# Optimization experiments

Hardware: AMD Instinct MI355X
Metric: run time of the kernel (lower is better)

## Reference

```python
import jax, jax.numpy as jnp
import numpy as np

B, T, S = 64, 32, 64          # batch, tgt_len, src_len
V, E, H, C = 32000, 512, 1024, 2048  # vocab, emb, hidden, context (2*d_model)


def setup_inputs() -> dict:
    key = jax.random.key(0)
    ks = jax.random.split(key, 16)
    g = lambda i, shape, s=0.05: jax.random.normal(ks[i], shape, jnp.float32) * s
    return dict(
        y=jax.random.randint(ks[0], (B, T), 0, V),
        context=g(1, (B, S, C), 1.0),
        context_mask=jnp.zeros((B, S), jnp.int32),  # 1 = padding
        hidden=g(2, (B, H), 1.0),
        emb=g(3, (V, E)),
        W_ih1=g(4, (3 * H, E)), W_hh1=g(5, (3 * H, H)),
        b_ih1=jnp.zeros((3 * H,), jnp.float32), b_hh1=jnp.zeros((3 * H,), jnp.float32),
        Wq=g(6, (H, H)), bq=jnp.zeros((H,), jnp.float32),
        Wk=g(7, (C, H)), v_attn=g(8, (H,)),
        W_ih2=g(9, (3 * H, C)), W_hh2=g(10, (3 * H, H)),
        b_ih2=jnp.zeros((3 * H,), jnp.float32), b_hh2=jnp.zeros((3 * H,), jnp.float32),
        Wi=g(11, (E, E)), bi=jnp.zeros((E,), jnp.float32),
        Wh=g(12, (E, H)), bh=jnp.zeros((E,), jnp.float32),
        Wc=g(13, (E, C)), bc=jnp.zeros((E,), jnp.float32),
    )


def gru_cell(x, h, W_ih, W_hh, b_ih, b_hh):
    gi = x @ W_ih.T + b_ih
    gh = h @ W_hh.T + b_hh
    i_r, i_z, i_n = jnp.split(gi, 3, axis=-1)
    h_r, h_z, h_n = jnp.split(gh, 3, axis=-1)
    r = jax.nn.sigmoid(i_r + h_r)
    z = jax.nn.sigmoid(i_z + h_z)
    n = jnp.tanh(i_n + r * h_n)
    return (1.0 - z) * n + z * h


def reference(y, context, context_mask, hidden, emb,
              W_ih1, W_hh1, b_ih1, b_hh1,
              Wq, bq, Wk, v_attn,
              W_ih2, W_hh2, b_ih2, b_hh2,
              Wi, bi, Wh, bh, Wc, bc):
    x = emb[y]                                        # [B,T,E]
    cache = jnp.einsum('bsc,ch->bsh', context, Wk)    # attention key cache
    pad = context_mask.astype(bool)
    neg = jnp.finfo(x.dtype).min

    def step(h, x_t):
        h1 = gru_cell(x_t, h, W_ih1, W_hh1, b_ih1, b_hh1)        # [B,H]
        q = h1 @ Wq + bq                                          # [B,H]
        scores = jnp.einsum('bsh,h->bs', jnp.tanh(q[:, None, :] + cache), v_attn)
        probs = jax.nn.softmax(jnp.where(pad, neg, scores), axis=-1)
        attn = jnp.einsum('bs,bsc->bc', probs, context)           # [B,C]
        h2 = gru_cell(attn, h1, W_ih2, W_hh2, b_ih2, b_hh2)
        return h2, (h2, attn)

    h_final, (out, attn) = jax.lax.scan(step, hidden, jnp.swapaxes(x, 0, 1))
    out = jnp.swapaxes(out, 0, 1)                     # [B,T,H]
    attn = jnp.swapaxes(attn, 0, 1)                   # [B,T,C]
    logits = jnp.tanh(x @ Wi.T + bi + out @ Wh.T + bh + attn @ Wc.T + bc)
    return logits, h_final
```

## Files before the change

kernel.cpp:

```cpp
#include <hip/hip_runtime.h>
#include <math.h>

#define B_ 64
#define T_ 32
#define S_ 64
#define E_ 512
#define H_ 1024
#define C_ 2048
#define G_ 3072
#define NBLK 256
#define FLSTR 16

typedef __bf16 bf16_t;
typedef bf16_t bf16x8 __attribute__((ext_vector_type(8)));
typedef float f32x4 __attribute__((ext_vector_type(4)));
typedef unsigned long long u64;

__device__ __forceinline__ float sigm_(float x) { return 1.f / (1.f + __expf(-x)); }
__device__ __forceinline__ float tanh_(float x) { return 1.f - 2.f / (__expf(2.f * x) + 1.f); }

__device__ __forceinline__ unsigned short bits_(bf16_t x)
{
    union { bf16_t b; unsigned short u; } c; c.b = x; return c.u;
}
__device__ __forceinline__ void astore_pair(bf16_t* p, bf16_t lo, bf16_t hi)
{
    unsigned u = (unsigned)bits_(lo) | ((unsigned)bits_(hi) << 16);
    __hip_atomic_store((unsigned*)p, u, __ATOMIC_RELAXED, __HIP_MEMORY_SCOPE_AGENT);
}
__device__ __forceinline__ void astore_f32(float* p, float v)
{
    union { float f; unsigned u; } c; c.f = v;
    __hip_atomic_store((unsigned*)p, c.u, __ATOMIC_RELAXED, __HIP_MEMORY_SCOPE_AGENT);
}
__device__ __forceinline__ void astore_2f32(float* p, float a, float b)
{
    union { float f[2]; u64 u; } c; c.f[0] = a; c.f[1] = b;
    __hip_atomic_store((u64*)p, c.u, __ATOMIC_RELAXED, __HIP_MEMORY_SCOPE_AGENT);
}

__device__ __forceinline__ void split8(const float* __restrict__ p, bf16x8& h, bf16x8& l)
{
    float4 a = *(const float4*)p;
    float4 b = *(const float4*)(p + 4);
    float v[8] = {a.x, a.y, a.z, a.w, b.x, b.y, b.z, b.w};
    #pragma unroll
    for (int q = 0; q < 8; ++q) {
        h[q] = (bf16_t)v[q];
        l[q] = (bf16_t)(v[q] - (float)h[q]);
    }
}

__global__ __launch_bounds__(256)
void embed_kernel(const int* __restrict__ y, const float* __restrict__ emb,
                  float* __restrict__ x)
{
    int i = blockIdx.x * 256 + threadIdx.x;
    int row = i / (E_ / 4);
    int e4  = i % (E_ / 4);
    const float4* src = (const float4*)(emb + (size_t)y[row] * E_);
    ((float4*)(x + (size_t)row * E_))[e4] = src[e4];
}

__global__ void transpose_kernel(const float* __restrict__ in, float* __restrict__ out,
                                 int R, int Ccols)
{
    __shared__ float t[32][33];
    int r0 = blockIdx.y * 32, c0 = blockIdx.x * 32;
    t[threadIdx.y][threadIdx.x] = in[(size_t)(r0 + threadIdx.y) * Ccols + c0 + threadIdx.x];
    __syncthreads();
    out[(size_t)(c0 + threadIdx.y) * R + r0 + threadIdx.x] = t[threadIdx.x][threadIdx.y];
}

__global__ __launch_bounds__(256)
void cvt_ctx(const float* __restrict__ in, bf16_t* __restrict__ out)
{
    int i = blockIdx.x * 256 + threadIdx.x;
    const float4* s4 = (const float4*)in + 2 * i;
    float4 a = s4[0], b = s4[1];
    bf16x8 o;
    o[0] = (bf16_t)a.x; o[1] = (bf16_t)a.y; o[2] = (bf16_t)a.z; o[3] = (bf16_t)a.w;
    o[4] = (bf16_t)b.x; o[5] = (bf16_t)b.y; o[6] = (bf16_t)b.z; o[7] = (bf16_t)b.w;
    ((bf16x8*)out)[i] = o;
}

#define LSTR 80

template<int ACCUM>
__global__ __launch_bounds__(256)
void sgemm(const float* __restrict__ A, const float* __restrict__ Wt,
           float* __restrict__ out, int N, int K)
{
    __shared__ char AH[128 * LSTR];
    __shared__ char AL[128 * LSTR];
    __shared__ char WH[128 * LSTR];
    __shared__ char WL[128 * LSTR];
    const int tid = threadIdx.x;
    const int lane = tid & 63, wave = tid >> 6;
    const int m0 = blockIdx.y * 128, n0 = blockIdx.x * 128;
    const int wm = (wave & 1) * 64, wn = (wave >> 1) * 64;
    const int l15 = lane & 15, l4 = lane >> 4;

    f32x4 acc[4][4] = {};

    for (int k0 = 0; k0 < K; k0 += 32) {
        #pragma unroll
        for (int p = 0; p < 2; ++p) {
            int e = tid + p * 256;
            int row = e >> 2, ch = e & 3;
            int off = row * LSTR + ch * 16;
            bf16x8 h, l;
            split8(A + (size_t)(m0 + row) * K + k0 + ch * 8, h, l);
            *(bf16x8*)(AH + off) = h; *(bf16x8*)(AL + off) = l;
            split8(Wt + (size_t)(n0 + row) * K + k0 + ch * 8, h, l);
            *(bf16x8*)(WH + off) = h; *(bf16x8*)(WL + off) = l;
        }
        __syncthreads();
        bf16x8 ah[4], al[4], wh[4], wl[4];
        #pragma unroll
        for (int i = 0; i < 4; ++i) {
            int off = (wm + i * 16 + l15) * LSTR + l4 * 16;
            ah[i] = *(const bf16x8*)(AH + off);
            al[i] = *(const bf16x8*)(AL + off);
        }
        #pragma unroll
        for (int j = 0; j < 4; ++j) {
            int off = (wn + j * 16 + l15) * LSTR + l4 * 16;
            wh[j] = *(const bf16x8*)(WH + off);
            wl[j] = *(const bf16x8*)(WL + off);
        }
        #pragma unroll
        for (int i = 0; i < 4; ++i)
            #pragma unroll
            for (int j = 0; j < 4; ++j) {
                acc[i][j] = __builtin_amdgcn_mfma_f32_16x16x32_bf16(ah[i], wh[j], acc[i][j], 0, 0, 0);
                acc[i][j] = __builtin_amdgcn_mfma_f32_16x16x32_bf16(ah[i], wl[j], acc[i][j], 0, 0, 0);
                acc[i][j] = __builtin_amdgcn_mfma_f32_16x16x32_bf16(al[i], wh[j], acc[i][j], 0, 0, 0);
            }
        __syncthreads();
    }

    #pragma unroll
    for (int i = 0; i < 4; ++i)
        #pragma unroll
        for (int j = 0; j < 4; ++j)
            #pragma unroll
            for (int r = 0; r < 4; ++r) {
                int m = m0 + wm + i * 16 + l4 * 4 + r;
                int n = n0 + wn + j * 16 + l15;
                if (ACCUM) out[(size_t)m * N + n] += acc[i][j][r];
                else       out[(size_t)m * N + n]  = acc[i][j][r];
            }
}

#define W1H_OFF 0
#define W1L_OFF 24576
#define W3H_OFF 49152
#define W2H_OFF 98304
#define W2L_OFF 131072
#define SMEM_BYTES 163840

__device__ __forceinline__ void gbar(unsigned* flags, unsigned* done,
                                     unsigned epoch, int blk, int tid)
{
    asm volatile("s_waitcnt vmcnt(0)" ::: "memory");
    __syncthreads();
    if (blk == 0) {
        if (tid > 0 && tid < NBLK) {
            while (__hip_atomic_load(&flags[tid * FLSTR], __ATOMIC_RELAXED,
                                     __HIP_MEMORY_SCOPE_AGENT) < epoch)
                __builtin_amdgcn_s_sleep(4);
        }
        __syncthreads();
        if (tid < 8)
            __hip_atomic_store(&done[tid * FLSTR], epoch, __ATOMIC_RELAXED,
                               __HIP_MEMORY_SCOPE_AGENT);
        __syncthreads();
    } else {
        if (tid == 0) {
            __hip_atomic_store(&flags[blk * FLSTR], epoch, __ATOMIC_RELAXED,
                               __HIP_MEMORY_SCOPE_AGENT);
            while (__hip_atomic_load(&done[(blk & 7) * FLSTR], __ATOMIC_RELAXED,
                                     __HIP_MEMORY_SCOPE_AGENT) < epoch)
                __builtin_amdgcn_s_sleep(4);
        }
        __syncthreads();
    }
}

__global__ __launch_bounds__(1024, 1)
void scan_kernel(
    const float* __restrict__ Whh1, const float* __restrict__ Whh2,
    const float* __restrict__ WqT,  const float* __restrict__ Wih2,
    const float* __restrict__ Xg,
    const float* __restrict__ b_ih1, const float* __restrict__ b_hh1,
    const float* __restrict__ b_ih2, const float* __restrict__ b_hh2,
    const float* __restrict__ bq,    const float* __restrict__ v_attn,
    const int*   __restrict__ cmask,
    const float* __restrict__ hidden,
    const float* __restrict__ cacheK, const bf16_t* __restrict__ ctxb,
    float* __restrict__ qgv, float* __restrict__ hf,
    bf16_t* __restrict__ h1H, bf16_t* __restrict__ h1L,
    float* __restrict__ attnseq, float* __restrict__ outseq,
    float* __restrict__ hfinal,
    float* __restrict__ scgv,
    unsigned* __restrict__ flags, unsigned* __restrict__ done)
{
    extern __shared__ char sm[];
    const int tid = threadIdx.x, blk = blockIdx.x;
    const int lane = tid & 63, wave = tid >> 6;
    const int l15 = lane & 15, l4 = lane >> 4;
    const int blk4 = blk * 4;
    const int ab  = blk & 63;
    const int aq  = blk >> 6;

    if (tid == 0) __builtin_amdgcn_fence(__ATOMIC_ACQUIRE, "agent");
    __syncthreads();

    for (int e = tid; e < 12 * 128; e += 1024) {
        int r = e >> 7, c = e & 127;
        bf16x8 h, l;
        split8(Whh1 + (size_t)((r >> 2) * 1024 + blk4 + (r & 3)) * 1024 + c * 8, h, l);
        int off = r * 2048 + ((c * 16) ^ ((r & 7) << 4));
        *(bf16x8*)(sm + W1H_OFF + off) = h;
        *(bf16x8*)(sm + W1L_OFF + off) = l;
    }
    for (int e = tid; e < 16 * 128; e += 1024) {
        int r = e >> 7, c = e & 127;
        const float* src = (r < 12)
            ? Whh2 + (size_t)((r >> 2) * 1024 + blk4 + (r & 3)) * 1024 + c * 8
            : WqT + (size_t)(blk4 + r - 12) * 1024 + c * 8;
        bf16x8 h, l;
        split8(src, h, l);
        int off = r * 2048 + ((c * 16) ^ ((r & 7) << 4));
        *(bf16x8*)(sm + W2H_OFF + off) = h;
        *(bf16x8*)(sm + W2L_OFF + off) = l;
    }
    for (int e = tid; e < 12 * 256; e += 1024) {
        int r = e >> 8, c = e & 255;
        bf16x8 h, l;
        split8(Wih2 + (size_t)((r >> 2) * 1024 + blk4 + (r & 3)) * 2048 + c * 8, h, l);
        *(bf16x8*)(sm + W3H_OFF + r * 4096 + ((c * 16) ^ ((r & 7) << 4))) = h;
    }

    const int j = blk4 + l15;
    if (wave < 4 && l15 < 4) {
        #pragma unroll
        for (int r2 = 0; r2 < 4; ++r2) {
            int b = wave * 16 + l4 * 4 + r2;
            hf[b * 1024 + j] = hidden[b * 1024 + j];
        }
    }

    float vreg[16], bqreg[16];
    #pragma unroll
    for (int i = 0; i < 16; ++i) {
        vreg[i]  = v_attn[lane + 64 * i];
        bqreg[i] = bq[lane + 64 * i];
    }

    float bi1r = 0, bi1z = 0, bi1n = 0, bh1r = 0, bh1z = 0, bh1n = 0;
    float bi2r = 0, bi2z = 0, bi2n = 0, bh2r = 0, bh2z = 0, bh2n = 0;
    if (wave < 4 && l15 < 4) {
        bi1r = b_ih1[j]; bi1z = b_ih1[1024 + j]; bi1n = b_ih1[2048 + j];
        bh1r = b_hh1[j]; bh1z = b_hh1[1024 + j]; bh1n = b_hh1[2048 + j];
        bi2r = b_ih2[j]; bi2z = b_ih2[1024 + j]; bi2n = b_ih2[2048 + j];
        bh2r = b_hh2[j]; bh2z = b_hh2[1024 + j]; bh2n = b_hh2[2048 + j];
    }

    unsigned epoch = 0;
    gbar(flags, done, ++epoch, blk, tid);

    float h1r_[4] = {0.f, 0.f, 0.f, 0.f};
    f32x4 acc1 = {0.f, 0.f, 0.f, 0.f};

    for (int t = 0; t < T_; ++t) {
        if (wave < 4) {
            f32x4 acc0 = {0.f, 0.f, 0.f, 0.f};
            const int brow = wave * 16 + l15;
            const float* asrc = (t == 0) ? hidden + (size_t)brow * 1024
                                         : outseq + ((size_t)brow * T_ + t - 1) * 1024;
            #pragma unroll 8
            for (int kk = 0; kk < 32; ++kk) {
                bf16x8 avh, avl;
                split8(asrc + kk * 32 + l4 * 8, avh, avl);
                int boff = (kk * 64 + l4 * 16) ^ ((l15 & 7) << 4);
                bf16x8 bvh = *(const bf16x8*)(sm + W1H_OFF + l15 * 2048 + boff);
                bf16x8 bvl = *(const bf16x8*)(sm + W1L_OFF + l15 * 2048 + boff);
                acc0 = __builtin_amdgcn_mfma_f32_16x16x32_bf16(avh, bvh, acc0, 0, 0, 0);
                acc0 = __builtin_amdgcn_mfma_f32_16x16x32_bf16(avl, bvh, acc0, 0, 0, 0);
                acc0 = __builtin_amdgcn_mfma_f32_16x16x32_bf16(avh, bvl, acc0, 0, 0, 0);
            }
            #pragma unroll
            for (int r2 = 0; r2 < 4; ++r2) {
                float gr = acc0[r2];
                float gz = __shfl(acc0[r2], (lane & 48) | (l15 + 4), 64);
                float gn = __shfl(acc0[r2], (lane & 48) | (l15 + 8), 64);
                float h1v = 0.f;
                int b = wave * 16 + l4 * 4 + r2;
                if (l15 < 4) {
                    const float* xg = Xg + ((size_t)b * T_ + t) * 3072;
                    float rr = sigm_(xg[j]          + bi1r + gr + bh1r);
                    float zz = sigm_(xg[1024 + j]   + bi1z + gz + bh1z);
                    float nn = tanh_(xg[2048 + j]   + bi1n + rr * (gn + bh1n));
                    h1v = (1.f - zz) * nn + zz * hf[b * 1024 + j];
                    h1r_[r2] = h1v;
                }
                float h1o = __shfl(h1v, lane + 1, 64);
                if (l15 < 4 && (l15 & 1) == 0) {
                    bf16_t hS = (bf16_t)h1v, hO = (bf16_t)h1o;
                    size_t vo = ((size_t)t * 64 + b) * 1024 + j;
                    astore_pair(h1H + vo, hS, hO);
                    astore_pair(h1L + vo,
                                (bf16_t)(h1v - (float)hS), (bf16_t)(h1o - (float)hO));
                }
            }
        }
        gbar(flags, done, ++epoch, blk, tid);

        if (wave < 4) {
            acc1 = (f32x4){0.f, 0.f, 0.f, 0.f};
            const int brow = wave * 16 + l15;
            const bf16_t* ah = h1H + ((size_t)t * 64 + brow) * 1024;
            const bf16_t* al = h1L + ((size_t)t * 64 + brow) * 1024;
            #pragma unroll 8
            for (int kk = 0; kk < 32; ++kk) {
                bf16x8 avh = *(const bf16x8*)(ah + kk * 32 + l4 * 8);
                bf16x8 avl = *(const bf16x8*)(al + kk * 32 + l4 * 8);
                int boff = (kk * 64 + l4 * 16) ^ ((l15 & 7) << 4);
                bf16x8 bvh = *(const bf16x8*)(sm + W2H_OFF + l15 * 2048 + boff);
                bf16x8 bvl = *(const bf16x8*)(sm + W2L_OFF + l15 * 2048 + boff);
                acc1 = __builtin_amdgcn_mfma_f32_16x16x32_bf16(avh, bvh, acc1, 0, 0, 0);
                acc1 = __builtin_amdgcn_mfma_f32_16x16x32_bf16(avl, bvh, acc1, 0, 0, 0);
                acc1 = __builtin_amdgcn_mfma_f32_16x16x32_bf16(avh, bvl, acc1, 0, 0, 0);
            }
            if (l15 >= 12) {
                int jq = blk4 + l15 - 12;
                #pragma unroll
                for (int r2 = 0; r2 < 4; ++r2)
                    astore_f32(&qgv[((size_t)t * 64 + (wave * 16 + l4 * 4 + r2)) * 1024 + jq],
                               acc1[r2]);
            }
        }
        gbar(flags, done, ++epoch, blk, tid);

        {
            int s = aq * 16 + wave;
            const float* qrow = qgv + ((size_t)t * 64 + ab) * 1024;
            const float* ck = cacheK + ((size_t)ab * 64 + s) * 1024;
            float sum = 0.f;
            #pragma unroll
            for (int i = 0; i < 16; ++i)
                sum += tanh_(qrow[lane + 64 * i] + bqreg[i] + ck[lane + 64 * i]) * vreg[i];
            #pragma unroll
            for (int off = 32; off; off >>= 1) sum += __shfl_down(sum, off, 64);
            if (lane == 0) astore_f32(&scgv[(size_t)t * 4096 + ab * 64 + s], sum);
        }
        gbar(flags, done, ++epoch, blk, tid);

        if (tid < 256) {
            const float* scrow = scgv + (size_t)t * 4096 + ab * 64;
            float v = (cmask[ab * 64 + lane] != 0) ? -3.4e38f : scrow[lane];
            float mx = v;
            #pragma unroll
            for (int off = 32; off; off >>= 1) mx = fmaxf(mx, __shfl_xor(mx, off, 64));
            float e = __expf(v - mx);
            float sden = e;
            #pragma unroll
            for (int off = 32; off; off >>= 1) sden += __shfl_xor(sden, off, 64);
            float prv = e / sden;

            int c = aq * 512 + tid * 2;
            const bf16_t* cb = ctxb + (size_t)ab * 64 * 2048 + c;
            float sum0 = 0.f, sum1 = 0.f;
            #pragma unroll 8
            for (int s = 0; s < 64; ++s) {
                float p = __shfl(prv, s, 64);
                bf16_t v0 = cb[(size_t)s * 2048];
                bf16_t v1 = cb[(size_t)s * 2048 + 1];
                sum0 += p * (float)v0;
                sum1 += p * (float)v1;
            }
            astore_2f32(attnseq + ((size_t)ab * T_ + t) * 2048 + c, sum0, sum1);
        }
        gbar(flags, done, ++epoch, blk, tid);

        if (wave < 4) {
            f32x4 acc3 = {0.f, 0.f, 0.f, 0.f};
            const int brow = wave * 16 + l15;
            const float* aptr = attnseq + ((size_t)brow * T_ + t) * 2048;
            #pragma unroll 8
            for (int kk = 0; kk < 64; ++kk) {
                bf16x8 avh, avl;
                split8(aptr + kk * 32 + l4 * 8, avh, avl);
                bf16x8 bvh = *(const bf16x8*)(sm + W3H_OFF + l15 * 4096 +
                                              ((kk * 64 + l4 * 16) ^ ((l15 & 7) << 4)));
                acc3 = __builtin_amdgcn_mfma_f32_16x16x32_bf16(avh, bvh, acc3, 0, 0, 0);
                acc3 = __builtin_amdgcn_mfma_f32_16x16x32_bf16(avl, bvh, acc3, 0, 0, 0);
            }
            #pragma unroll
            for (int r2 = 0; r2 < 4; ++r2) {
                float ir  = acc3[r2];
                float iz  = __shfl(acc3[r2], (lane & 48) | (l15 + 4), 64);
                float in2 = __shfl(acc3[r2], (lane & 48) | (l15 + 8), 64);
                float hr  = acc1[r2];
                float hz  = __shfl(acc1[r2], (lane & 48) | (l15 + 4), 64);
                float hn  = __shfl(acc1[r2], (lane & 48) | (l15 + 8), 64);
                int b = wave * 16 + l4 * 4 + r2;
                if (l15 < 4) {
                    float rr = sigm_(ir + bi2r + hr + bh2r);
                    float zz = sigm_(iz + bi2z + hz + bh2z);
                    float nn = tanh_(in2 + bi2n + rr * (hn + bh2n));
                    float h2 = (1.f - zz) * nn + zz * h1r_[r2];
                    hf[b * 1024 + j] = h2;
                    astore_f32(&outseq[((size_t)b * T_ + t) * 1024 + j], h2);
                    if (t == T_ - 1) hfinal[b * 1024 + j] = h2;
                }
            }
        }
        gbar(flags, done, ++epoch, blk, tid);
    }
}

__global__ __launch_bounds__(256)
void final_kernel(const float* __restrict__ Lacc,
                  const float* __restrict__ bi, const float* __restrict__ bh,
                  const float* __restrict__ bc, float* __restrict__ out)
{
    int i = blockIdx.x * 256 + threadIdx.x;
    int e = i & 511;
    out[i] = tanh_(Lacc[i] + bi[e] + bh[e] + bc[e]);
}

extern "C" void kernel_launch(void* const* d_in, const int* in_sizes, int n_in,
                              void* d_out, int out_size, void* d_ws, size_t ws_size,
                              hipStream_t stream)
{
    const int*   y       = (const int*)  d_in[0];
    const float* context = (const float*)d_in[1];
    const int*   cmask   = (const int*)  d_in[2];
    const float* hidden  = (const float*)d_in[3];
    const float* emb     = (const float*)d_in[4];
    const float* W_ih1   = (const float*)d_in[5];
    const float* W_hh1   = (const float*)d_in[6];
    const float* b_ih1   = (const float*)d_in[7];
    const float* b_hh1   = (const float*)d_in[8];
    const float* Wq      = (const float*)d_in[9];
    const float* bq      = (const float*)d_in[10];
    const float* Wk      = (const float*)d_in[11];
    const float* v_attn  = (const float*)d_in[12];
    const float* W_ih2   = (const float*)d_in[13];
    const float* W_hh2   = (const float*)d_in[14];
    const float* b_ih2   = (const float*)d_in[15];
    const float* b_hh2   = (const float*)d_in[16];
    const float* Wi      = (const float*)d_in[17];
    const float* bi      = (const float*)d_in[18];
    const float* Wh      = (const float*)d_in[19];
    const float* bh      = (const float*)d_in[20];
    const float* Wc      = (const float*)d_in[21];
    const float* bc      = (const float*)d_in[22];

    char* ws = (char*)d_ws;
    size_t o = 0;
    auto alloc = [&](size_t bytes) { char* p = ws + o; o += (bytes + 255) & ~(size_t)255; return p; };
    unsigned* flags = (unsigned*)alloc(NBLK * FLSTR * 4);
    unsigned* done  = (unsigned*)alloc(8 * FLSTR * 4);
    float*  x       = (float*) alloc((size_t)2048 * 512 * 4);
    float*  WkT     = (float*) alloc((size_t)1024 * 2048 * 4);
    float*  WqT     = (float*) alloc((size_t)1024 * 1024 * 4);
    bf16_t* ctxb    = (bf16_t*)alloc((size_t)4096 * 2048 * 2);
    float*  Xg      = (float*) alloc((size_t)2048 * 3072 * 4);
    float*  Lacc    = (float*) alloc((size_t)2048 * 512 * 4);
    float*  cacheK  = (float*) alloc((size_t)4096 * 1024 * 4);
    float*  qgv     = (float*) alloc((size_t)T_ * 64 * 1024 * 4);
    float*  hf      = (float*) alloc((size_t)64 * 1024 * 4);
    bf16_t* h1H     = (bf16_t*)alloc((size_t)T_ * 64 * 1024 * 2);
    bf16_t* h1L     = (bf16_t*)alloc((size_t)T_ * 64 * 1024 * 2);
    float*  attnseq = (float*) alloc((size_t)2048 * 2048 * 4);
    float*  outseq  = (float*) alloc((size_t)2048 * 1024 * 4);
    float*  scgv    = (float*) alloc((size_t)T_ * 64 * 64 * 4);

    hipMemsetAsync(flags, 0, (NBLK * FLSTR + 8 * FLSTR) * 4, stream);

    embed_kernel<<<(B_*T_*E_/4 + 255)/256, 256, 0, stream>>>(y, emb, x);
    transpose_kernel<<<dim3(1024/32, 2048/32), dim3(32,32), 0, stream>>>(Wk, WkT, 2048, 1024);
    transpose_kernel<<<dim3(1024/32, 1024/32), dim3(32,32), 0, stream>>>(Wq, WqT, 1024, 1024);
    cvt_ctx<<<(4096*2048/8)/256, 256, 0, stream>>>(context, ctxb);

    sgemm<0><<<dim3(G_/128, 16), 256, 0, stream>>>(x, W_ih1, Xg, G_, E_);
    sgemm<0><<<dim3(E_/128, 16), 256, 0, stream>>>(x, Wi, Lacc, E_, E_);
    sgemm<0><<<dim3(H_/128, 32), 256, 0, stream>>>(context, WkT, cacheK, H_, C_);

    hipFuncSetAttribute((const void*)scan_kernel, hipFuncAttributeMaxDynamicSharedMemorySize, SMEM_BYTES);
    scan_kernel<<<NBLK, 1024, SMEM_BYTES, stream>>>(
        W_hh1, W_hh2, WqT, W_ih2, Xg,
        b_ih1, b_hh1, b_ih2, b_hh2, bq, v_attn, cmask, hidden, cacheK, ctxb,
        qgv, hf, h1H, h1L, attnseq, outseq,
        (float*)d_out + (size_t)B_ * T_ * E_, scgv, flags, done);

    sgemm<1><<<dim3(E_/128, 16), 256, 0, stream>>>(outseq, Wh, Lacc, E_, H_);
    sgemm<1><<<dim3(E_/128, 16), 256, 0, stream>>>(attnseq, Wc, Lacc, E_, C_);

    final_kernel<<<(B_*T_*E_)/256, 256, 0, stream>>>(Lacc, bi, bh, bc, (float*)d_out);
}
```

Before: 3.423 ms.

## Cache attention keys and context slices in registers; permute input-gate layout for scan

The persistent scan kernel now loads each block's cacheK row and its bf16 context column slice into registers once, before the time loop, instead of re-reading them from global memory every step. The attention-context reduction is spread over all 1024 threads, with each pair splitting the source positions and combining via a shuffle. The input-gate GEMM writes its output in a per-block, per-time-step layout so the GRU gate reads are contiguous. The launch bounds change from (1024, 1) to (1024, 4), which may force lower register limits and cause spills given the added register arrays.

```diff
diff --git a/kernel.cpp b/kernel.cpp
--- a/kernel.cpp
+++ b/kernel.cpp
@@ -33,11 +33,6 @@
     union { float f; unsigned u; } c; c.f = v;
     __hip_atomic_store((unsigned*)p, c.u, __ATOMIC_RELAXED, __HIP_MEMORY_SCOPE_AGENT);
 }
-__device__ __forceinline__ void astore_2f32(float* p, float a, float b)
-{
-    union { float f[2]; u64 u; } c; c.f[0] = a; c.f[1] = b;
-    __hip_atomic_store((u64*)p, c.u, __ATOMIC_RELAXED, __HIP_MEMORY_SCOPE_AGENT);
-}
 
 __device__ __forceinline__ void split8(const float* __restrict__ p, bf16x8& h, bf16x8& l)
 {
@@ -86,7 +81,7 @@
 
 #define LSTR 80
 
-template<int ACCUM>
+template<int ACCUM, int PERM>
 __global__ __launch_bounds__(256)
 void sgemm(const float* __restrict__ A, const float* __restrict__ Wt,
            float* __restrict__ out, int N, int K)
@@ -148,8 +143,17 @@
             for (int r = 0; r < 4; ++r) {
                 int m = m0 + wm + i * 16 + l4 * 4 + r;
                 int n = n0 + wn + j * 16 + l15;
-                if (ACCUM) out[(size_t)m * N + n] += acc[i][j][r];
-                else       out[(size_t)m * N + n]  = acc[i][j][r];
+                if (PERM) {
+                    int b = m >> 5, t = m & 31;
+                    int gate = n >> 10, jj = n & 1023;
+                    size_t dst = (((size_t)(jj >> 2) * 32 + t) * 64 + b) * 12
+                                 + gate * 4 + (jj & 3);
+                    out[dst] = acc[i][j][r];
+                } else if (ACCUM) {
+                    out[(size_t)m * N + n] += acc[i][j][r];
+                } else {
+                    out[(size_t)m * N + n] = acc[i][j][r];
+                }
             }
 }
 
@@ -188,11 +192,11 @@
     }
 }
 
-__global__ __launch_bounds__(1024, 1)
+__global__ __launch_bounds__(1024, 4)
 void scan_kernel(
     const float* __restrict__ Whh1, const float* __restrict__ Whh2,
     const float* __restrict__ WqT,  const float* __restrict__ Wih2,
-    const float* __restrict__ Xg,
+    const float* __restrict__ xg2,
     const float* __restrict__ b_ih1, const float* __restrict__ b_hh1,
     const float* __restrict__ b_ih2, const float* __restrict__ b_hh2,
     const float* __restrict__ bq,    const float* __restrict__ v_attn,
@@ -257,6 +261,24 @@
     for (int i = 0; i < 16; ++i) {
         vreg[i]  = v_attn[lane + 64 * i];
         bqreg[i] = bq[lane + 64 * i];
+    }
+    float ckreg[16];
+    {
+        const float* ck = cacheK + ((size_t)ab * 64 + aq * 16 + wave) * 1024;
+        #pragma unroll
+        for (int i = 0; i < 16; ++i) ckreg[i] = ck[lane + 64 * i];
+    }
+    const int cmy = aq * 512 + (tid >> 1);
+    const int sbase = (tid & 1) * 32;
+    unsigned cr[16];
+    {
+        const bf16_t* cb = ctxb + ((size_t)ab * 64 + sbase) * 2048 + cmy;
+        #pragma unroll
+        for (int q = 0; q < 16; ++q) {
+            unsigned lo = bits_(cb[(size_t)(2 * q) * 2048]);
+            unsigned hi = bits_(cb[(size_t)(2 * q + 1) * 2048]);
+            cr[q] = lo | (hi << 16);
+        }
     }
 
     float bi1r = 0, bi1z = 0, bi1n = 0, bh1r = 0, bh1z = 0, bh1n = 0;
@@ -291,6 +313,7 @@
                 acc0 = __builtin_amdgcn_mfma_f32_16x16x32_bf16(avl, bvh, acc0, 0, 0, 0);
                 acc0 = __builtin_amdgcn_mfma_f32_16x16x32_bf16(avh, bvl, acc0, 0, 0, 0);
             }
+            const float* xg = xg2 + (((size_t)blk * 32 + t) * 64) * 12;
             #pragma unroll
             for (int r2 = 0; r2 < 4; ++r2) {
                 float gr = acc0[r2];
@@ -299,10 +322,9 @@
                 float h1v = 0.f;
                 int b = wave * 16 + l4 * 4 + r2;
                 if (l15 < 4) {
-                    const float* xg = Xg + ((size_t)b * T_ + t) * 3072;
-                    float rr = sigm_(xg[j]          + bi1r + gr + bh1r);
-                    float zz = sigm_(xg[1024 + j]   + bi1z + gz + bh1z);
-                    float nn = tanh_(xg[2048 + j]   + bi1n + rr * (gn + bh1n));
+                    float rr = sigm_(xg[b * 12 + l15]     + bi1r + gr + bh1r);
+                    float zz = sigm_(xg[b * 12 + 4 + l15] + bi1z + gz + bh1z);
+                    float nn = tanh_(xg[b * 12 + 8 + l15] + bi1n + rr * (gn + bh1n));
                     h1v = (1.f - zz) * nn + zz * hf[b * 1024 + j];
                     h1r_[r2] = h1v;
                 }
@@ -345,20 +367,18 @@
         gbar(flags, done, ++epoch, blk, tid);
 
         {
-            int s = aq * 16 + wave;
             const float* qrow = qgv + ((size_t)t * 64 + ab) * 1024;
-            const float* ck = cacheK + ((size_t)ab * 64 + s) * 1024;
             float sum = 0.f;
             #pragma unroll
             for (int i = 0; i < 16; ++i)
-                sum += tanh_(qrow[lane + 64 * i] + bqreg[i] + ck[lane + 64 * i]) * vreg[i];
+                sum += tanh_(qrow[lane + 64 * i] + bqreg[i] + ckreg[i]) * vreg[i];
             #pragma unroll
             for (int off = 32; off; off >>= 1) sum += __shfl_down(sum, off, 64);
-            if (lane == 0) astore_f32(&scgv[(size_t)t * 4096 + ab * 64 + s], sum);
+            if (lane == 0) astore_f32(&scgv[(size_t)t * 4096 + ab * 64 + aq * 16 + wave], sum);
         }
         gbar(flags, done, ++epoch, blk, tid);
 
-        if (tid < 256) {
+        {
             const float* scrow = scgv + (size_t)t * 4096 + ab * 64;
             float v = (cmask[ab * 64 + lane] != 0) ? -3.4e38f : scrow[lane];
             float mx = v;
@@ -370,18 +390,17 @@
             for (int off = 32; off; off >>= 1) sden += __shfl_xor(sden, off, 64);
             float prv = e / sden;
 
-            int c = aq * 512 + tid * 2;
-            const bf16_t* cb = ctxb + (size_t)ab * 64 * 2048 + c;
-            float sum0 = 0.f, sum1 = 0.f;
-            #pragma unroll 8
-            for (int s = 0; s < 64; ++s) {
-                float p = __shfl(prv, s, 64);
-                bf16_t v0 = cb[(size_t)s * 2048];
-                bf16_t v1 = cb[(size_t)s * 2048 + 1];
-                sum0 += p * (float)v0;
-                sum1 += p * (float)v1;
-            }
-            astore_2f32(attnseq + ((size_t)ab * T_ + t) * 2048 + c, sum0, sum1);
+            float sum = 0.f;
+            #pragma unroll
+            for (int q = 0; q < 16; ++q) {
+                float p0 = __shfl(prv, sbase + 2 * q, 64);
+                float p1 = __shfl(prv, sbase + 2 * q + 1, 64);
+                sum += p0 * __uint_as_float(cr[q] << 16);
+                sum += p1 * __uint_as_float(cr[q] & 0xffff0000u);
+            }
+            sum += __shfl_xor(sum, 1, 64);
+            if ((tid & 1) == 0)
+                astore_f32(attnseq + ((size_t)ab * T_ + t) * 2048 + cmy, sum);
         }
         gbar(flags, done, ++epoch, blk, tid);
 
@@ -469,7 +488,7 @@
     float*  WkT     = (float*) alloc((size_t)1024 * 2048 * 4);
     float*  WqT     = (float*) alloc((size_t)1024 * 1024 * 4);
     bf16_t* ctxb    = (bf16_t*)alloc((size_t)4096 * 2048 * 2);
-    float*  Xg      = (float*) alloc((size_t)2048 * 3072 * 4);
+    float*  xg2     = (float*) alloc((size_t)2048 * 3072 * 4);
     float*  Lacc    = (float*) alloc((size_t)2048 * 512 * 4);
     float*  cacheK  = (float*) alloc((size_t)4096 * 1024 * 4);
     float*  qgv     = (float*) alloc((size_t)T_ * 64 * 1024 * 4);
@@ -487,19 +506,19 @@
     transpose_kernel<<<dim3(1024/32, 1024/32), dim3(32,32), 0, stream>>>(Wq, WqT, 1024, 1024);
     cvt_ctx<<<(4096*2048/8)/256, 256, 0, stream>>>(context, ctxb);
 
-    sgemm<0><<<dim3(G_/128, 16), 256, 0, stream>>>(x, W_ih1, Xg, G_, E_);
-    sgemm<0><<<dim3(E_/128, 16), 256, 0, stream>>>(x, Wi, Lacc, E_, E_);
-    sgemm<0><<<dim3(H_/128, 32), 256, 0, stream>>>(context, WkT, cacheK, H_, C_);
+    sgemm<0, 1><<<dim3(G_/128, 16), 256, 0, stream>>>(x, W_ih1, xg2, G_, E_);
+    sgemm<0, 0><<<dim3(E_/128, 16), 256, 0, stream>>>(x, Wi, Lacc, E_, E_);
+    sgemm<0, 0><<<dim3(H_/128, 32), 256, 0, stream>>>(context, WkT, cacheK, H_, C_);
 
     hipFuncSetAttribute((const void*)scan_kernel, hipFuncAttributeMaxDynamicSharedMemorySize, SMEM_BYTES);
     scan_kernel<<<NBLK, 1024, SMEM_BYTES, stream>>>(
-        W_hh1, W_hh2, WqT, W_ih2, Xg,
+        W_hh1, W_hh2, WqT, W_ih2, xg2,
         b_ih1, b_hh1, b_ih2, b_hh2, bq, v_attn, cmask, hidden, cacheK, ctxb,
         qgv, hf, h1H, h1L, attnseq, outseq,
         (float*)d_out + (size_t)B_ * T_ * E_, scgv, flags, done);
 
-    sgemm<1><<<dim3(E_/128, 16), 256, 0, stream>>>(outseq, Wh, Lacc, E_, H_);
-    sgemm<1><<<dim3(E_/128, 16), 256, 0, stream>>>(attnseq, Wc, Lacc, E_, C_);
+    sgemm<1, 0><<<dim3(E_/128, 16), 256, 0, stream>>>(outseq, Wh, Lacc, E_, H_);
+    sgemm<1, 0><<<dim3(E_/128, 16), 256, 0, stream>>>(attnseq, Wc, Lacc, E_, C_);
 
     final_kernel<<<(B_*T_*E_)/256, 256, 0, stream>>>(Lacc, bi, bh, bc, (float*)d_out);
 }
```

After: 3.134 ms. 8.5% less time.
